# Optimization experiments

Measured on AMD Instinct MI355X. Metric: run time of the kernel, lower is better.

## Reference

```python
import jax, jax.numpy as jnp
import numpy as np

# regular 3x3 kernel grid: row0 = dy (i-1), row1 = dx (j-1), k = 3*i + j
RY = jnp.array([-1., -1., -1., 0., 0., 0., 1., 1., 1.], dtype=jnp.float32)
RX = jnp.array([-1., 0., 1., -1., 0., 1., -1., 0., 1.], dtype=jnp.float32)


def conv2d(x, w, b):
    # 3x3, stride 1, pad 1, NCHW/OIHW
    out = jax.lax.conv_general_dilated(
        x, w, window_strides=(1, 1), padding=((1, 1), (1, 1)),
        dimension_numbers=('NCHW', 'OIHW', 'NCHW'))
    return out + b[None, :, None, None]


def group_norm(x, gamma, beta, num_groups, eps=1e-5):
    N, C, H, W = x.shape
    xg = x.reshape(N, num_groups, C // num_groups, H, W)
    mu = xg.mean(axis=(2, 3, 4), keepdims=True)
    var = xg.var(axis=(2, 3, 4), keepdims=True)
    xn = ((xg - mu) * jax.lax.rsqrt(var + eps)).reshape(N, C, H, W)
    return xn * gamma[None, :, None, None] + beta[None, :, None, None]


def build_offset(tm, tr):
    # tm: [N,4,H,W] per-pixel 2x2 affine [[m00,m01],[m10,m11]]; tr: [N,2,H,W] (ty, tx)
    m00, m01, m10, m11 = tm[:, 0], tm[:, 1], tm[:, 2], tm[:, 3]  # [N,H,W]
    ry = RY[None, :, None, None]
    rx = RX[None, :, None, None]
    # offset = M @ R - R, plus translation broadcast to all 9 points
    dy = m00[:, None] * ry + m01[:, None] * rx - ry + tr[:, 0:1]  # [N,9,H,W]
    dx = m10[:, None] * ry + m11[:, None] * rx - rx + tr[:, 1:2]  # [N,9,H,W]
    return dy, dx


def bilinear_sample(img, py, px):
    # img: [N,C,H,W]; py, px: [N,K,H,W] sampling locations; zero padding outside
    N, C, H, W = img.shape
    K = py.shape[1]
    y0f = jnp.floor(py)
    x0f = jnp.floor(px)
    wy1 = py - y0f
    wx1 = px - x0f
    wy0 = 1.0 - wy1
    wx0 = 1.0 - wx1
    y0 = y0f.astype(jnp.int32)
    x0 = x0f.astype(jnp.int32)
    img_flat = img.reshape(N, C, H * W)

    def gather(yi, xi):
        valid = ((yi >= 0) & (yi < H) & (xi >= 0) & (xi < W)).astype(img.dtype)
        idx = jnp.clip(yi, 0, H - 1) * W + jnp.clip(xi, 0, W - 1)  # [N,K,H,W]
        flat = idx.reshape(N, 1, K * H * W)
        vals = jnp.take_along_axis(img_flat, jnp.broadcast_to(flat, (N, C, K * H * W)), axis=2)
        return vals.reshape(N, C, K, H, W) * valid[:, None]

    v00 = gather(y0, x0)
    v01 = gather(y0, x0 + 1)
    v10 = gather(y0 + 1, x0)
    v11 = gather(y0 + 1, x0 + 1)
    return (v00 * (wy0 * wx0)[:, None] + v01 * (wy0 * wx1)[:, None]
            + v10 * (wy1 * wx0)[:, None] + v11 * (wy1 * wx1)[:, None])


def deform_conv(x, dy, dx, w, pad=1, dil=1):
    # x: [N,Cin,H,W]; dy,dx: [N,9,H,W]; w: [Cout,Cin,3,3]; stride 1
    N, C, H, W = x.shape
    k = jnp.arange(9)
    ki = (k // 3).astype(x.dtype)[None, :, None, None]
    kj = (k % 3).astype(x.dtype)[None, :, None, None]
    hh = jnp.arange(H, dtype=x.dtype)[None, None, :, None]
    ww = jnp.arange(W, dtype=x.dtype)[None, None, None, :]
    py = hh - pad + dil * ki + dy  # [N,9,H,W]
    px = ww - pad + dil * kj + dx
    sampled = bilinear_sample(x, py, px)  # [N,C,9,H,W]
    return jnp.einsum('nckhw,ock->nohw', sampled, w.reshape(w.shape[0], C, 9))


def setup_inputs() -> dict:
    key = jax.random.key(0)
    ks = jax.random.split(key, 16)
    N, C, H, W = 4, 256, 64, 64
    x = jax.random.normal(ks[0], (N, C, H, W), jnp.float32)
    def p(k, shape, s):
        return jax.random.normal(k, shape, jnp.float32) * s
    s_off = 0.01                       # small STN heads -> modest offsets
    s_dc = 1.0 / np.sqrt(C * 9.0)      # deform-conv fan-in init
    return {
        'x': x,
        'w_tm1': p(ks[1], (4, C, 3, 3), s_off), 'b_tm1': jnp.zeros((4,), jnp.float32),
        'w_tr1': p(ks[2], (2, C, 3, 3), s_off), 'b_tr1': jnp.zeros((2,), jnp.float32),
        'w_dc1': p(ks[3], (C, C, 3, 3), s_dc),
        'g1': jnp.ones((C,), jnp.float32), 'be1': jnp.zeros((C,), jnp.float32),
        'w_tm2': p(ks[4], (4, C, 3, 3), s_off), 'b_tm2': jnp.zeros((4,), jnp.float32),
        'w_tr2': p(ks[5], (2, C, 3, 3), s_off), 'b_tr2': jnp.zeros((2,), jnp.float32),
        'w_dc2': p(ks[6], (C, C, 3, 3), s_dc),
        'g2': jnp.ones((C,), jnp.float32), 'be2': jnp.zeros((C,), jnp.float32),
    }


def reference(x, w_tm1, b_tm1, w_tr1, b_tr1, w_dc1, g1, be1,
              w_tm2, b_tm2, w_tr2, b_tr2, w_dc2, g2, be2):
    GROUPS = 32
    residual = x
    dy1, dx1 = build_offset(conv2d(x, w_tm1, b_tm1), conv2d(x, w_tr1, b_tr1))
    out = deform_conv(x, dy1, dx1, w_dc1)
    out = jax.nn.relu(group_norm(out, g1, be1, GROUPS))
    dy2, dx2 = build_offset(conv2d(out, w_tm2, b_tm2), conv2d(out, w_tr2, b_tr2))
    out = deform_conv(out, dy2, dx2, w_dc2)
    out = group_norm(out, g2, be2, GROUPS)
    return jax.nn.relu(out + residual)
```

## Files before the change

### kernel.cpp

```cpp
#include <hip/hip_runtime.h>


typedef unsigned int u32;
typedef unsigned short u16;
typedef __attribute__((ext_vector_type(8))) short bf16x8;
typedef __attribute__((ext_vector_type(4))) float floatx4;

#define HW 4096
#define CHW 1048576

static __device__ __forceinline__ float bf2f(u16 u) {
    union { u32 i; float f; } c; c.i = ((u32)u) << 16; return c.f;
}
static __device__ __forceinline__ u16 f2bf(float f) {
    union { float f; u32 i; } c; c.f = f;
    u32 x = c.i;
    return (u16)((x + 0x7FFFu + ((x >> 16) & 1u)) >> 16);
}
static __device__ __forceinline__ u32 cvtpk(float a, float b) {
    u32 r;
    asm("v_cvt_pk_bf16_f32 %0, %1, %2" : "=v"(r) : "v"(a), "v"(b));
    return r;
}
static __device__ __forceinline__ void lbar() {
    __builtin_amdgcn_sched_barrier(0);
    asm volatile("s_waitcnt lgkmcnt(0)" ::: "memory");
    __builtin_amdgcn_s_barrier();
    __builtin_amdgcn_sched_barrier(0);
}
static __device__ __forceinline__ float loadv(const void* p, long i, int f32) {
    return f32 ? ((const float*)p)[i] : bf2f(((const u16*)p)[i]);
}
static __device__ __forceinline__ int sniff_f32(const u32* __restrict__ xw) {
    int cnt = 0;
    #pragma unroll
    for (int s = 0; s < 16; ++s) {
        union { u32 i; float f; } c;
        c.i = xw[s * 131 + 7];
        float a = fabsf(c.f);
        if (a > 1e-8f && a < 1e4f) ++cnt;
    }
    return (cnt >= 8) ? 1 : 0;
}

__global__ __launch_bounds__(256) void k_prep_all(
    const void* __restrict__ x,
    const void* __restrict__ wdc1, const void* __restrict__ wdc2,
    const void* __restrict__ wtm1, const void* __restrict__ wtr1,
    const void* __restrict__ wtm2, const void* __restrict__ wtr2,
    u16* __restrict__ xT, u16* __restrict__ wTg1, u16* __restrict__ wTg2,
    u16* __restrict__ wT61, u16* __restrict__ wT62)
{
    __shared__ u16 T[64 * 258];
    const int f32 = sniff_f32((const u32*)x);
    const int b = blockIdx.x;
    const int tid = threadIdx.x;

    if (b < 256) {
        const int n = b >> 6, h = b & 63;
        const long sb = (long)n * CHW + (h << 6);
        const int cb = tid >> 3;
        const int w0 = (tid & 7) << 3;
        if (f32) {
            const float* xp = (const float*)x;
            for (int it = 0; it < 8; ++it) {
                int c = (it << 5) + cb;
                const float* pr = xp + sb + (long)c * HW + w0;
                float4 a = ((const float4*)pr)[0];
                float4 d = ((const float4*)pr)[1];
                T[(w0 + 0) * 258 + c] = f2bf(a.x);
                T[(w0 + 1) * 258 + c] = f2bf(a.y);
                T[(w0 + 2) * 258 + c] = f2bf(a.z);
                T[(w0 + 3) * 258 + c] = f2bf(a.w);
                T[(w0 + 4) * 258 + c] = f2bf(d.x);
                T[(w0 + 5) * 258 + c] = f2bf(d.y);
                T[(w0 + 6) * 258 + c] = f2bf(d.z);
                T[(w0 + 7) * 258 + c] = f2bf(d.w);
            }
        } else {
            const u16* xp = (const u16*)x;
            for (int it = 0; it < 8; ++it) {
                int c = (it << 5) + cb;
                uint4 v = *(const uint4*)(xp + sb + (long)c * HW + w0);
                u32 ws[4] = {v.x, v.y, v.z, v.w};
                #pragma unroll
                for (int q = 0; q < 4; ++q) {
                    T[(w0 + 2 * q + 0) * 258 + c] = (u16)(ws[q] & 0xFFFFu);
                    T[(w0 + 2 * q + 1) * 258 + c] = (u16)(ws[q] >> 16);
                }
            }
        }
        __syncthreads();
        const int w = tid >> 2, cq = tid & 3;
        const u32* Tr = (const u32*)T;
        u16* ob = xT + (long)n * CHW + (long)((h << 6) + w) * 256 + cq * 64;
        #pragma unroll
        for (int s = 0; s < 8; ++s) {
            uint4 o;
            o.x = Tr[129 * w + 32 * cq + 4 * s + 0];
            o.y = Tr[129 * w + 32 * cq + 4 * s + 1];
            o.z = Tr[129 * w + 32 * cq + 4 * s + 2];
            o.w = Tr[129 * w + 32 * cq + 4 * s + 3];
            *(uint4*)&ob[s * 8] = o;
        }
    } else if (b < 2560) {
        const int r2 = (b >= 1408);
        const void* wdc = r2 ? wdc2 : wdc1;
        u16* wTg = r2 ? wTg2 : wTg1;
        int idx2 = (b - (r2 ? 1408 : 256)) * 256 + tid;
        int cp = idx2 & 15;
        int o  = (idx2 >> 4) & 255;
        int q  = idx2 >> 12;
        int k  = q >> 3;
        int c0 = ((q & 7) << 5) + (cp << 1);
        long s0 = (long)o * 2304 + c0 * 9 + k;
        ((u32*)wTg)[idx2] = cvtpk(loadv(wdc, s0, f32), loadv(wdc, s0 + 9, f32));
    } else {
        const int r2 = (b >= 2704);
        const void* wtm = r2 ? wtm2 : wtm1;
        const void* wtr = r2 ? wtr2 : wtr1;
        u16* wT6 = r2 ? wT62 : wT61;
        int i = (b - (r2 ? 2704 : 2560)) * 256 + tid;
        int q  = i >> 9;
        int o  = (i >> 5) & 15;
        int cc = i & 31;
        int k  = q >> 3;
        int c  = ((q & 7) << 5) + cc;
        float v = 0.f;
        if (o < 4)      v = loadv(wtm, (long)o * 2304 + c * 9 + k, f32);
        else if (o < 6) v = loadv(wtr, (long)(o - 4) * 2304 + c * 9 + k, f32);
        wT6[i] = f2bf(v);
    }
}

__global__ __launch_bounds__(1024, 4) void k_deform(
    const u16* __restrict__ srcT, const u16* __restrict__ wTg,
    const u16* __restrict__ wT6,
    const void* __restrict__ b_tm, const void* __restrict__ b_tr,
    const u32* __restrict__ xw,
    u16* __restrict__ raw, float* __restrict__ pstats)
{
    __shared__ __align__(16) char shm[65536];
    __shared__ float tl[6 * 64];
    __shared__ int   g_y0[576];
    __shared__ int   g_x0[576];
    __shared__ float g_wy[576];
    __shared__ float g_wx[576];

    const int tid = threadIdx.x;
    const int bid = blockIdx.x;
    const int n = bid >> 6, h = bid & 63;
    const int lane = tid & 63;
    const int quad = lane >> 4;
    const int l16  = lane & 15;
    const int wv   = tid >> 6;
    const long nbase = (long)n * CHW;
    const u16* sp = srcT + nbase;

    {
        float (*red)[64][17] = (float (*)[64][17])shm;
        if (wv < 8) {
            floatx4 acc6[4];
            #pragma unroll
            for (int j = 0; j < 4; ++j) acc6[j] = (floatx4){0.f, 0.f, 0.f, 0.f};
            for (int qi = 0; qi < 9; ++qi) {
                const int q = wv * 9 + qi;
                const int k = q >> 3, cb = q & 7;
                const int ky = k / 3, kx = k % 3;
                const int row = h + ky - 1;
                const bool rv = (row >= 0) && (row < 64);
                bf16x8 av = *(const bf16x8*)&wT6[(((q << 4) + l16) << 5) + (quad << 3)];
                #pragma unroll
                for (int j = 0; j < 4; ++j) {
                    int psrc = (j << 4) + l16 + kx - 1;
                    bf16x8 bv = {0, 0, 0, 0, 0, 0, 0, 0};
                    if (rv && psrc >= 0 && psrc < 64)
                        bv = *(const bf16x8*)&sp[(((long)(row << 6) + psrc) << 8) + (cb << 5) + (quad << 3)];
                    acc6[j] = __builtin_amdgcn_mfma_f32_16x16x32_bf16(av, bv, acc6[j], 0, 0, 0);
                }
            }
            #pragma unroll
            for (int j = 0; j < 4; ++j)
                #pragma unroll
                for (int r = 0; r < 4; ++r)
                    red[wv][(j << 4) + l16][(quad << 2) + r] = acc6[j][r];
        }
        __syncthreads();
        if (tid < 384) {
            const int o = tid >> 6, px = tid & 63;
            float s = 0.f;
            #pragma unroll
            for (int v = 0; v < 8; ++v) s += red[v][px][o];
            const int f32 = sniff_f32(xw);
            float bias = (o < 4) ? loadv(b_tm, o, f32) : loadv(b_tr, o - 4, f32);
            tl[o * 64 + px] = s + bias;
        }
        __syncthreads();
    }

    if (tid < 576) {
        int i = tid;
        int k = i >> 6, ww2 = i & 63;
        float m00 = tl[ww2],        m01 = tl[64 + ww2];
        float m10 = tl[128 + ww2],  m11 = tl[192 + ww2];
        float tr0 = tl[256 + ww2],  tr1 = tl[320 + ww2];
        float ry = (float)(k / 3) - 1.f;
        float rx = (float)(k % 3) - 1.f;
        float dy = m00 * ry + m01 * rx - ry + tr0;
        float dx = m10 * ry + m11 * rx - rx + tr1;
        float py = (float)h + ry + dy;
        float px = (float)ww2 + rx + dx;
        float y0f = floorf(py), x0f = floorf(px);
        g_y0[i] = (int)y0f; g_x0[i] = (int)x0f;
        g_wy[i] = py - y0f; g_wx[i] = px - x0f;
    }
    __syncthreads();

    const int px   = tid >> 4;
    const int slot = tid & 15;
    const int kh   = wv >> 3;
    const int o0   = (wv & 7) << 5;
    const u32 xw_s = (u32)((px  & 7) << 2);
    const u32 xsw  = (u32)((l16 & 7) << 2);
    const u32 q4x  = (u32)(quad << 2);
    const u32 kh64 = (u32)(kh << 6);

    u32* Sl = (u32*)shm;

    floatx4 acc[2][4];
    #pragma unroll
    for (int a = 0; a < 2; ++a)
        #pragma unroll
        for (int g = 0; g < 4; ++g) acc[a][g] = (floatx4){0.f, 0.f, 0.f, 0.f};

    const int wlane = ((o0 + l16) << 5) + (quad << 3);
    const u16* wk = wTg + (kh << 15);

    u32 o00, o01, o10, o11;
    float cw00, cw01, cw10, cw11;
    const char* spb = (const char*)sp + (slot << 4);

    auto mkptr = [&](int k) {
        int gi = (k << 6) + px;
        int y0 = g_y0[gi], x0 = g_x0[gi];
        int yc0 = min(max(y0, 0), 63),     yc1 = min(max(y0 + 1, 0), 63);
        int xc0 = min(max(x0, 0), 63),     xc1 = min(max(x0 + 1, 0), 63);
        o00 = (u32)(((yc0 << 6) + xc0) << 9);
        o01 = (u32)(((yc0 << 6) + xc1) << 9);
        o10 = (u32)(((yc1 << 6) + xc0) << 9);
        o11 = (u32)(((yc1 << 6) + xc1) << 9);
    };
    auto mkcw = [&](int k) {
        int gi = (k << 6) + px;
        int y0 = g_y0[gi], x0 = g_x0[gi];
        float wy1 = g_wy[gi], wx1 = g_wx[gi];
        float wy0 = 1.f - wy1, wx0 = 1.f - wx1;
        bool yv0 = (y0 >= 0) && (y0 < 64);
        bool yv1 = (y0 >= -1) && (y0 < 63);
        bool xv0 = (x0 >= 0) && (x0 < 64);
        bool xv1 = (x0 >= -1) && (x0 < 63);
        cw00 = (yv0 && xv0) ? wy0 * wx0 : 0.f;
        cw01 = (yv0 && xv1) ? wy0 * wx1 : 0.f;
        cw10 = (yv1 && xv0) ? wy1 * wx0 : 0.f;
        cw11 = (yv1 && xv1) ? wy1 * wx1 : 0.f;
    };

    uint4 GA, GB, GC, GD, HA, HB, HC, HD;
    auto GATHER = [&]() {
        GA = *(const uint4*)(spb + o00);  HA = *(const uint4*)(spb + o00 + 256);
        GB = *(const uint4*)(spb + o01);  HB = *(const uint4*)(spb + o01 + 256);
        GC = *(const uint4*)(spb + o10);  HC = *(const uint4*)(spb + o10 + 256);
        GD = *(const uint4*)(spb + o11);  HD = *(const uint4*)(spb + o11 + 256);
    };

    bf16x8 W0[4], W1[4];

#define BIL(a, b, c, d) cvtpk( \
    fmaf(cw00, bf2f((u16)(a)), fmaf(cw01, bf2f((u16)(b)), \
    fmaf(cw10, bf2f((u16)(c)), cw11 * bf2f((u16)(d))))), \
    fmaf(cw00, bf2f((u16)((a) >> 16)), fmaf(cw01, bf2f((u16)((b) >> 16)), \
    fmaf(cw10, bf2f((u16)((c) >> 16)), cw11 * bf2f((u16)((d) >> 16))))))

    mkptr(0); GATHER();
    W0[0] = *(const bf16x8*)(wk + wlane);
    W1[0] = *(const bf16x8*)(wk + wlane + 512);
    W0[1] = *(const bf16x8*)(wk + 8192 + wlane);
    W1[1] = *(const bf16x8*)(wk + 8192 + wlane + 512);

    for (int k = 0; k < 9; ++k) {
        const int buf = k & 1;
        mkcw(k);
        uint4 v0 = make_uint4(BIL(GA.x, GB.x, GC.x, GD.x), BIL(GA.y, GB.y, GC.y, GD.y),
                              BIL(GA.z, GB.z, GC.z, GD.z), BIL(GA.w, GB.w, GC.w, GD.w));
        uint4 v1 = make_uint4(BIL(HA.x, HB.x, HC.x, HD.x), BIL(HA.y, HB.y, HC.y, HD.y),
                              BIL(HA.z, HB.z, HC.z, HD.z), BIL(HA.w, HB.w, HC.w, HD.w));
        u32* wp = &Sl[((u32)(buf << 13)) + ((u32)(px << 7)) + (((u32)(slot << 2)) ^ xw_s)];
        *(uint4*)wp = v0;
        *(uint4*)(wp + 64) = v1;
        if (k < 8) { mkptr(k + 1); GATHER(); }
        lbar();
        const u32* sb = &Sl[(u32)(buf << 13)];
        #pragma unroll
        for (int c = 0; c < 4; ++c) {
            const u32 offc = (((kh64 + (u32)(c << 4))) | q4x) ^ xsw;
            bf16x8 b0 = *(const bf16x8*)(sb + ((u32)(( 0 + l16) << 7)) + offc);
            bf16x8 b1 = *(const bf16x8*)(sb + ((u32)((16 + l16) << 7)) + offc);
            bf16x8 b2 = *(const bf16x8*)(sb + ((u32)((32 + l16) << 7)) + offc);
            bf16x8 b3 = *(const bf16x8*)(sb + ((u32)((48 + l16) << 7)) + offc);
            if (k < 8 || c < 2) {
                const int tc = c + 2;
                const u16* wb = wk + ((tc & 3) + ((tc >> 2) << 3)) * 8192;
                W0[tc & 3] = *(const bf16x8*)(wb + wlane);
                W1[tc & 3] = *(const bf16x8*)(wb + wlane + 512);
            }
            acc[0][0] = __builtin_amdgcn_mfma_f32_16x16x32_bf16(W0[c], b0, acc[0][0], 0, 0, 0);
            acc[0][1] = __builtin_amdgcn_mfma_f32_16x16x32_bf16(W0[c], b1, acc[0][1], 0, 0, 0);
            acc[0][2] = __builtin_amdgcn_mfma_f32_16x16x32_bf16(W0[c], b2, acc[0][2], 0, 0, 0);
            acc[0][3] = __builtin_amdgcn_mfma_f32_16x16x32_bf16(W0[c], b3, acc[0][3], 0, 0, 0);
            acc[1][0] = __builtin_amdgcn_mfma_f32_16x16x32_bf16(W1[c], b0, acc[1][0], 0, 0, 0);
            acc[1][1] = __builtin_amdgcn_mfma_f32_16x16x32_bf16(W1[c], b1, acc[1][1], 0, 0, 0);
            acc[1][2] = __builtin_amdgcn_mfma_f32_16x16x32_bf16(W1[c], b2, acc[1][2], 0, 0, 0);
            acc[1][3] = __builtin_amdgcn_mfma_f32_16x16x32_bf16(W1[c], b3, acc[1][3], 0, 0, 0);
        }
        wk += 65536;
    }
#undef BIL

    __syncthreads();
    {
        float* ms = (float*)shm;
        if (kh == 1) {
            #pragma unroll
            for (int a = 0; a < 2; ++a)
                #pragma unroll
                for (int g = 0; g < 4; ++g)
                    *(floatx4*)&ms[((((wv & 7) << 3) + (a << 2) + g) << 8) + (lane << 2)] = acc[a][g];
        }
        __syncthreads();
        if (kh == 0) {
            #pragma unroll
            for (int a = 0; a < 2; ++a)
                #pragma unroll
                for (int g = 0; g < 4; ++g) {
                    floatx4 t = *(const floatx4*)&ms[((((wv & 7) << 3) + (a << 2) + g) << 8) + (lane << 2)];
                    acc[a][g] += t;
                }
        }
    }

    if (kh == 0) {
        #pragma unroll
        for (int a = 0; a < 2; ++a) {
            float s1 = 0.f, s2 = 0.f;
            #pragma unroll
            for (int g = 0; g < 4; ++g)
                #pragma unroll
                for (int r = 0; r < 4; ++r) {
                    float v = acc[a][g][r];
                    s1 += v; s2 += v * v;
                }
            #pragma unroll
            for (int off = 1; off <= 16; off <<= 1) {
                s1 += __shfl_xor(s1, off, 64);
                s2 += __shfl_xor(s2, off, 64);
            }
            if ((lane & 31) == 0) {
                int gg = (o0 >> 3) + (a << 1) + (lane >> 5);
                pstats[((long)bid << 6) + (gg << 1)]     = s1;
                pstats[((long)bid << 6) + (gg << 1) + 1] = s2;
            }
        }

        #pragma unroll
        for (int a = 0; a < 2; ++a)
            #pragma unroll
            for (int g = 0; g < 4; ++g)
                #pragma unroll
                for (int r = 0; r < 4; ++r) {
                    int o = o0 + (a << 4) + (quad << 2) + r;
                    raw[nbase + ((long)o << 12) + (h << 6) + (g << 4) + l16]
                        = f2bf(acc[a][g][r]);
                }
    }
}

__global__ __launch_bounds__(256) void k_gn_relu(
    const u16* __restrict__ raw, const float* __restrict__ pstats,
    const void* __restrict__ gamma, const void* __restrict__ beta,
    const u32* __restrict__ xw,
    u16* __restrict__ out1)
{
    __shared__ u16 T[64 * 258];
    __shared__ float sred[4][64];
    __shared__ float sl[64];
    const int f32 = sniff_f32(xw);
    const int bid = blockIdx.x;
    const int n = bid >> 6, h = bid & 63;
    const int tid = threadIdx.x;

    {
        const int v = tid & 63, part = tid >> 6;
        float a = 0.f;
        for (int j = part * 16; j < part * 16 + 16; ++j)
            a += pstats[(((long)n * 64 + j) << 6) + v];
        sred[part][v] = a;
        __syncthreads();
        if (tid < 64) sl[tid] = sred[0][tid] + sred[1][tid] + sred[2][tid] + sred[3][tid];
        __syncthreads();
    }

    const u16* rb = raw + (long)n * CHW + (h << 6);
    const int cb = tid >> 3;
    const int w0 = (tid & 7) << 3;
    for (int it = 0; it < 8; ++it) {
        int c = (it << 5) + cb;
        int g = c >> 3;
        float mean = sl[g * 2] * (1.f / 32768.f);
        float var  = sl[g * 2 + 1] * (1.f / 32768.f) - mean * mean;
        float rstd = rsqrtf(var + 1e-5f);
        float ga = loadv(gamma, c, f32) * rstd;
        float be = loadv(beta, c, f32) - mean * ga;
        uint4 v = *(const uint4*)(rb + (long)c * HW + w0);
        u32 ws[4] = {v.x, v.y, v.z, v.w};
        #pragma unroll
        for (int q = 0; q < 4; ++q) {
            float a = fmaxf(fmaf(bf2f((u16)(ws[q] & 0xFFFFu)), ga, be), 0.f);
            float b = fmaxf(fmaf(bf2f((u16)(ws[q] >> 16)),     ga, be), 0.f);
            T[(w0 + 2 * q + 0) * 258 + c] = f2bf(a);
            T[(w0 + 2 * q + 1) * 258 + c] = f2bf(b);
        }
    }
    __syncthreads();
    const int w = tid >> 2, cq = tid & 3;
    const u32* Tr = (const u32*)T;
    u16* ob = out1 + (long)n * CHW + (long)((h << 6) + w) * 256 + cq * 64;
    #pragma unroll
    for (int s = 0; s < 8; ++s) {
        uint4 o;
        o.x = Tr[129 * w + 32 * cq + 4 * s + 0];
        o.y = Tr[129 * w + 32 * cq + 4 * s + 1];
        o.z = Tr[129 * w + 32 * cq + 4 * s + 2];
        o.w = Tr[129 * w + 32 * cq + 4 * s + 3];
        *(uint4*)&ob[s * 8] = o;
    }
}

__global__ __launch_bounds__(256) void k_gn_final(
    const u16* __restrict__ raw, const float* __restrict__ pstats,
    const void* __restrict__ gamma, const void* __restrict__ beta,
    const void* __restrict__ x,
    void* __restrict__ outp)
{
    __shared__ float rr[256];
    const int f32 = sniff_f32((const u32*)x);
    const int tid = threadIdx.x;
    const long e0 = ((long)blockIdx.x) << 11;
    const int n = (int)(e0 >> 20);
    const int c0 = (int)((e0 >> 12) & 255);
    const int g = c0 >> 3;

    {
        int j = tid & 127, sv = tid >> 7;
        rr[tid] = (j < 64) ? pstats[(((long)n * 64 + j) << 6) + (g << 1) + sv] : 0.f;
        __syncthreads();
        #pragma unroll
        for (int s = 64; s >= 1; s >>= 1) {
            if ((tid & 127) < s) rr[tid] += rr[tid + s];
            __syncthreads();
        }
    }
    float mean = rr[0] * (1.f / 32768.f);
    float var  = rr[128] * (1.f / 32768.f) - mean * mean;
    float rstd = rsqrtf(var + 1e-5f);

    const long i = blockIdx.x * 256 + tid;
    const long e = i << 3;
    const int c = (int)((e >> 12) & 255);
    float ga = loadv(gamma, c, f32) * rstd;
    float be = loadv(beta, c, f32) - mean * ga;
    uint4 p = ((const uint4*)raw)[i];
    u32 ww[4] = {p.x, p.y, p.z, p.w};
    float v[8];
    #pragma unroll
    for (int q = 0; q < 4; ++q) {
        v[2 * q + 0] = fmaxf(fmaf(bf2f((u16)(ww[q] & 0xFFFFu)), ga, be) + loadv(x, e + 2 * q + 0, f32), 0.f);
        v[2 * q + 1] = fmaxf(fmaf(bf2f((u16)(ww[q] >> 16)),     ga, be) + loadv(x, e + 2 * q + 1, f32), 0.f);
    }
    if (f32) {
        float4* op = (float4*)((float*)outp + e);
        op[0] = make_float4(v[0], v[1], v[2], v[3]);
        op[1] = make_float4(v[4], v[5], v[6], v[7]);
    } else {
        uint4 o;
        o.x = cvtpk(v[0], v[1]);
        o.y = cvtpk(v[2], v[3]);
        o.z = cvtpk(v[4], v[5]);
        o.w = cvtpk(v[6], v[7]);
        ((uint4*)outp)[i] = o;
    }
}

extern "C" void kernel_launch(void* const* d_in, const int* in_sizes, int n_in,
                              void* d_out, int out_size, void* d_ws, size_t ws_size,
                              hipStream_t stream) {
    const void* x     = d_in[0];
    const void* w_tm1 = d_in[1];
    const void* b_tm1 = d_in[2];
    const void* w_tr1 = d_in[3];
    const void* b_tr1 = d_in[4];
    const void* w_dc1 = d_in[5];
    const void* g1    = d_in[6];
    const void* be1   = d_in[7];
    const void* w_tm2 = d_in[8];
    const void* b_tm2 = d_in[9];
    const void* w_tr2 = d_in[10];
    const void* b_tr2 = d_in[11];
    const void* w_dc2 = d_in[12];
    const void* g2    = d_in[13];
    const void* be2   = d_in[14];

    char* wsb = (char*)d_ws;
    u16*   xT     = (u16*)wsb;
    u16*   raw    = (u16*)(wsb + 8388608);
    u16*   wTg1   = (u16*)(wsb + 16777216);
    u16*   wTg2   = (u16*)(wsb + 17956864);
    u16*   wT61   = (u16*)(wsb + 19136512);
    u16*   wT62   = (u16*)(wsb + 19210240);
    float* pstats = (float*)(wsb + 19283968);
    u16*   out1   = xT;
    const u32* xw = (const u32*)x;

    k_prep_all<<<2848, 256, 0, stream>>>(x, w_dc1, w_dc2, w_tm1, w_tr1, w_tm2, w_tr2,
                                         xT, wTg1, wTg2, wT61, wT62);
    k_deform  <<<256, 1024, 0, stream>>>(xT, wTg1, wT61, b_tm1, b_tr1, xw, raw, pstats);
    k_gn_relu <<<256, 256, 0, stream>>>(raw, pstats, g1, be1, xw, out1);
    k_deform  <<<256, 1024, 0, stream>>>(out1, wTg2, wT62, b_tm2, b_tr2, xw, raw, pstats);
    k_gn_final<<<2048, 256, 0, stream>>>(raw, pstats, g2, be2, x, d_out);
}
```

Measured before the change: 214.3 us.

## Write first deform output in NHWC and simplify GN-ReLU to elementwise pass

The first deform-conv pass now writes its raw output directly in channel-last layout using packed bf16 stores. This lets the GroupNorm+ReLU kernel become a flat elementwise kernel over 2048 blocks with no LDS transpose. The input transpose in the prep kernel is also split into half-row blocks to raise the block count. The aim is to remove the shared-memory transpose cost and improve parallelism, at the cost of an extra layout flag and scattered 8-byte stores from the deform epilogue.

```diff
diff --git a/kernel.cpp b/kernel.cpp
--- a/kernel.cpp
+++ b/kernel.cpp
@@ -51,63 +51,56 @@
     u16* __restrict__ xT, u16* __restrict__ wTg1, u16* __restrict__ wTg2,
     u16* __restrict__ wT61, u16* __restrict__ wT62)
 {
-    __shared__ u16 T[64 * 258];
+    __shared__ u16 T[32 * 258];
     const int f32 = sniff_f32((const u32*)x);
     const int b = blockIdx.x;
     const int tid = threadIdx.x;
 
-    if (b < 256) {
-        const int n = b >> 6, h = b & 63;
-        const long sb = (long)n * CHW + (h << 6);
+    if (b < 512) {
+        const int n = b >> 7, h = (b >> 1) & 63, half = b & 1;
+        const int wbase = half << 5;
+        const long sb = (long)n * CHW + (h << 6) + wbase;
         const int cb = tid >> 3;
-        const int w0 = (tid & 7) << 3;
+        const int w0 = (tid & 7) << 2;
         if (f32) {
             const float* xp = (const float*)x;
             for (int it = 0; it < 8; ++it) {
                 int c = (it << 5) + cb;
-                const float* pr = xp + sb + (long)c * HW + w0;
-                float4 a = ((const float4*)pr)[0];
-                float4 d = ((const float4*)pr)[1];
+                float4 a = *(const float4*)(xp + sb + (long)c * HW + w0);
                 T[(w0 + 0) * 258 + c] = f2bf(a.x);
                 T[(w0 + 1) * 258 + c] = f2bf(a.y);
                 T[(w0 + 2) * 258 + c] = f2bf(a.z);
                 T[(w0 + 3) * 258 + c] = f2bf(a.w);
-                T[(w0 + 4) * 258 + c] = f2bf(d.x);
-                T[(w0 + 5) * 258 + c] = f2bf(d.y);
-                T[(w0 + 6) * 258 + c] = f2bf(d.z);
-                T[(w0 + 7) * 258 + c] = f2bf(d.w);
             }
         } else {
             const u16* xp = (const u16*)x;
             for (int it = 0; it < 8; ++it) {
                 int c = (it << 5) + cb;
-                uint4 v = *(const uint4*)(xp + sb + (long)c * HW + w0);
-                u32 ws[4] = {v.x, v.y, v.z, v.w};
-                #pragma unroll
-                for (int q = 0; q < 4; ++q) {
-                    T[(w0 + 2 * q + 0) * 258 + c] = (u16)(ws[q] & 0xFFFFu);
-                    T[(w0 + 2 * q + 1) * 258 + c] = (u16)(ws[q] >> 16);
-                }
+                uint2 v = *(const uint2*)(xp + sb + (long)c * HW + w0);
+                T[(w0 + 0) * 258 + c] = (u16)(v.x & 0xFFFFu);
+                T[(w0 + 1) * 258 + c] = (u16)(v.x >> 16);
+                T[(w0 + 2) * 258 + c] = (u16)(v.y & 0xFFFFu);
+                T[(w0 + 3) * 258 + c] = (u16)(v.y >> 16);
             }
         }
         __syncthreads();
-        const int w = tid >> 2, cq = tid & 3;
+        const int w = tid >> 3, cq = tid & 7;
         const u32* Tr = (const u32*)T;
-        u16* ob = xT + (long)n * CHW + (long)((h << 6) + w) * 256 + cq * 64;
+        u16* ob = xT + (long)n * CHW + (long)((h << 6) + wbase + w) * 256 + cq * 32;
         #pragma unroll
-        for (int s = 0; s < 8; ++s) {
+        for (int s = 0; s < 4; ++s) {
             uint4 o;
-            o.x = Tr[129 * w + 32 * cq + 4 * s + 0];
-            o.y = Tr[129 * w + 32 * cq + 4 * s + 1];
-            o.z = Tr[129 * w + 32 * cq + 4 * s + 2];
-            o.w = Tr[129 * w + 32 * cq + 4 * s + 3];
+            o.x = Tr[129 * w + 16 * cq + 4 * s + 0];
+            o.y = Tr[129 * w + 16 * cq + 4 * s + 1];
+            o.z = Tr[129 * w + 16 * cq + 4 * s + 2];
+            o.w = Tr[129 * w + 16 * cq + 4 * s + 3];
             *(uint4*)&ob[s * 8] = o;
         }
-    } else if (b < 2560) {
-        const int r2 = (b >= 1408);
+    } else if (b < 2816) {
+        const int r2 = (b >= 1664);
         const void* wdc = r2 ? wdc2 : wdc1;
         u16* wTg = r2 ? wTg2 : wTg1;
-        int idx2 = (b - (r2 ? 1408 : 256)) * 256 + tid;
+        int idx2 = (b - (r2 ? 1664 : 512)) * 256 + tid;
         int cp = idx2 & 15;
         int o  = (idx2 >> 4) & 255;
         int q  = idx2 >> 12;
@@ -116,11 +109,11 @@
         long s0 = (long)o * 2304 + c0 * 9 + k;
         ((u32*)wTg)[idx2] = cvtpk(loadv(wdc, s0, f32), loadv(wdc, s0 + 9, f32));
     } else {
-        const int r2 = (b >= 2704);
+        const int r2 = (b >= 2960);
         const void* wtm = r2 ? wtm2 : wtm1;
         const void* wtr = r2 ? wtr2 : wtr1;
         u16* wT6 = r2 ? wT62 : wT61;
-        int i = (b - (r2 ? 2704 : 2560)) * 256 + tid;
+        int i = (b - (r2 ? 2960 : 2816)) * 256 + tid;
         int q  = i >> 9;
         int o  = (i >> 5) & 15;
         int cc = i & 31;
@@ -138,7 +131,7 @@
     const u16* __restrict__ wT6,
     const void* __restrict__ b_tm, const void* __restrict__ b_tr,
     const u32* __restrict__ xw,
-    u16* __restrict__ raw, float* __restrict__ pstats)
+    u16* __restrict__ raw, float* __restrict__ pstats, const int nhwc)
 {
     __shared__ __align__(16) char shm[65536];
     __shared__ float tl[6 * 64];
@@ -371,16 +364,30 @@
             }
         }
 
-        #pragma unroll
-        for (int a = 0; a < 2; ++a)
-            #pragma unroll
-            for (int g = 0; g < 4; ++g)
-                #pragma unroll
-                for (int r = 0; r < 4; ++r) {
-                    int o = o0 + (a << 4) + (quad << 2) + r;
-                    raw[nbase + ((long)o << 12) + (h << 6) + (g << 4) + l16]
-                        = f2bf(acc[a][g][r]);
+        if (nhwc) {
+            u16* rb = raw + nbase + ((long)h << 14);
+            #pragma unroll
+            for (int a = 0; a < 2; ++a)
+                #pragma unroll
+                for (int g = 0; g < 4; ++g) {
+                    int pxe = (g << 4) + l16;
+                    int o = o0 + (a << 4) + (quad << 2);
+                    u32 lo = cvtpk(acc[a][g][0], acc[a][g][1]);
+                    u32 hi = cvtpk(acc[a][g][2], acc[a][g][3]);
+                    *(uint2*)&rb[(pxe << 8) + o] = make_uint2(lo, hi);
                 }
+        } else {
+            #pragma unroll
+            for (int a = 0; a < 2; ++a)
+                #pragma unroll
+                for (int g = 0; g < 4; ++g)
+                    #pragma unroll
+                    for (int r = 0; r < 4; ++r) {
+                        int o = o0 + (a << 4) + (quad << 2) + r;
+                        raw[nbase + ((long)o << 12) + (h << 6) + (g << 4) + l16]
+                            = f2bf(acc[a][g][r]);
+                    }
+        }
     }
 }
 
@@ -390,13 +397,12 @@
     const u32* __restrict__ xw,
     u16* __restrict__ out1)
 {
-    __shared__ u16 T[64 * 258];
     __shared__ float sred[4][64];
     __shared__ float sl[64];
     const int f32 = sniff_f32(xw);
+    const int tid = threadIdx.x;
     const int bid = blockIdx.x;
-    const int n = bid >> 6, h = bid & 63;
-    const int tid = threadIdx.x;
+    const int n = bid >> 9;
 
     {
         const int v = tid & 63, part = tid >> 6;
@@ -409,40 +415,47 @@
         __syncthreads();
     }
 
-    const u16* rb = raw + (long)n * CHW + (h << 6);
-    const int cb = tid >> 3;
-    const int w0 = (tid & 7) << 3;
-    for (int it = 0; it < 8; ++it) {
-        int c = (it << 5) + cb;
-        int g = c >> 3;
-        float mean = sl[g * 2] * (1.f / 32768.f);
-        float var  = sl[g * 2 + 1] * (1.f / 32768.f) - mean * mean;
-        float rstd = rsqrtf(var + 1e-5f);
-        float ga = loadv(gamma, c, f32) * rstd;
-        float be = loadv(beta, c, f32) - mean * ga;
-        uint4 v = *(const uint4*)(rb + (long)c * HW + w0);
-        u32 ws[4] = {v.x, v.y, v.z, v.w};
+    const long i = (((long)bid) << 8) + tid;
+    const int c0 = (int)((i << 3) & 255);
+    const int g = c0 >> 3;
+    float mean = sl[g * 2] * (1.f / 32768.f);
+    float var  = sl[g * 2 + 1] * (1.f / 32768.f) - mean * mean;
+    float rstd = rsqrtf(var + 1e-5f);
+
+    float ga[8], be[8];
+    if (f32) {
+        float4 a0 = ((const float4*)gamma)[c0 >> 2];
+        float4 a1 = ((const float4*)gamma)[(c0 >> 2) + 1];
+        float4 b0 = ((const float4*)beta)[c0 >> 2];
+        float4 b1 = ((const float4*)beta)[(c0 >> 2) + 1];
+        ga[0]=a0.x; ga[1]=a0.y; ga[2]=a0.z; ga[3]=a0.w;
+        ga[4]=a1.x; ga[5]=a1.y; ga[6]=a1.z; ga[7]=a1.w;
+        be[0]=b0.x; be[1]=b0.y; be[2]=b0.z; be[3]=b0.w;
+        be[4]=b1.x; be[5]=b1.y; be[6]=b1.z; be[7]=b1.w;
+    } else {
+        uint4 av = ((const uint4*)gamma)[c0 >> 3];
+        uint4 bv = ((const uint4*)beta)[c0 >> 3];
+        u32 aw[4] = {av.x, av.y, av.z, av.w};
+        u32 bw[4] = {bv.x, bv.y, bv.z, bv.w};
         #pragma unroll
         for (int q = 0; q < 4; ++q) {
-            float a = fmaxf(fmaf(bf2f((u16)(ws[q] & 0xFFFFu)), ga, be), 0.f);
-            float b = fmaxf(fmaf(bf2f((u16)(ws[q] >> 16)),     ga, be), 0.f);
-            T[(w0 + 2 * q + 0) * 258 + c] = f2bf(a);
-            T[(w0 + 2 * q + 1) * 258 + c] = f2bf(b);
-        }
-    }
-    __syncthreads();
-    const int w = tid >> 2, cq = tid & 3;
-    const u32* Tr = (const u32*)T;
-    u16* ob = out1 + (long)n * CHW + (long)((h << 6) + w) * 256 + cq * 64;
+            ga[2*q] = bf2f((u16)(aw[q] & 0xFFFFu)); ga[2*q+1] = bf2f((u16)(aw[q] >> 16));
+            be[2*q] = bf2f((u16)(bw[q] & 0xFFFFu)); be[2*q+1] = bf2f((u16)(bw[q] >> 16));
+        }
+    }
+
+    uint4 p = ((const uint4*)raw)[i];
+    u32 ww[4] = {p.x, p.y, p.z, p.w};
+    u32 o[4];
     #pragma unroll
-    for (int s = 0; s < 8; ++s) {
-        uint4 o;
-        o.x = Tr[129 * w + 32 * cq + 4 * s + 0];
-        o.y = Tr[129 * w + 32 * cq + 4 * s + 1];
-        o.z = Tr[129 * w + 32 * cq + 4 * s + 2];
-        o.w = Tr[129 * w + 32 * cq + 4 * s + 3];
-        *(uint4*)&ob[s * 8] = o;
-    }
+    for (int q = 0; q < 4; ++q) {
+        float g0 = ga[2*q] * rstd,     g1 = ga[2*q+1] * rstd;
+        float b0 = be[2*q] - mean*g0,  b1 = be[2*q+1] - mean*g1;
+        float a = fmaxf(fmaf(bf2f((u16)(ww[q] & 0xFFFFu)), g0, b0), 0.f);
+        float b = fmaxf(fmaf(bf2f((u16)(ww[q] >> 16)),     g1, b1), 0.f);
+        o[q] = cvtpk(a, b);
+    }
+    ((uint4*)out1)[i] = make_uint4(o[0], o[1], o[2], o[3]);
 }
 
 __global__ __launch_bounds__(256) void k_gn_final(
@@ -530,10 +543,10 @@
     u16*   out1   = xT;
     const u32* xw = (const u32*)x;
 
-    k_prep_all<<<2848, 256, 0, stream>>>(x, w_dc1, w_dc2, w_tm1, w_tr1, w_tm2, w_tr2,
+    k_prep_all<<<3104, 256, 0, stream>>>(x, w_dc1, w_dc2, w_tm1, w_tr1, w_tm2, w_tr2,
                                          xT, wTg1, wTg2, wT61, wT62);
-    k_deform  <<<256, 1024, 0, stream>>>(xT, wTg1, wT61, b_tm1, b_tr1, xw, raw, pstats);
-    k_gn_relu <<<256, 256, 0, stream>>>(raw, pstats, g1, be1, xw, out1);
-    k_deform  <<<256, 1024, 0, stream>>>(out1, wTg2, wT62, b_tm2, b_tr2, xw, raw, pstats);
+    k_deform  <<<256, 1024, 0, stream>>>(xT, wTg1, wT61, b_tm1, b_tr1, xw, raw, pstats, 1);
+    k_gn_relu <<<2048, 256, 0, stream>>>(raw, pstats, g1, be1, xw, out1);
+    k_deform  <<<256, 1024, 0, stream>>>(out1, wTg2, wT62, b_tm2, b_tr2, xw, raw, pstats, 0);
     k_gn_final<<<2048, 256, 0, stream>>>(raw, pstats, g2, be2, x, d_out);
 }
```

Result: no change. 211.6 us (-1.3%).
